# Optimization experiments

Hardware: AMD Instinct MI355X
Metric: run time of the kernel (lower is better)

Reference implementation:

```python
import jax, jax.numpy as jnp
import numpy as np

B, H, W, C = 8, 64, 64, 128
L = H * W
NH = 4
HD = C // NH
SCALE = HD ** -0.5
WIN = 8
SHIFT = 4
DEPTH = 2
K = 3
N = WIN * WIN
NW = (H // WIN) * (W // WIN)


def _rel_pos_index(win):
    coords = np.stack(np.meshgrid(np.arange(win), np.arange(win), indexing='ij'))
    cf = coords.reshape(2, -1)
    rel = (cf[:, :, None] - cf[:, None, :]).transpose(1, 2, 0).copy()
    rel[:, :, 0] += win - 1
    rel[:, :, 1] += win - 1
    rel[:, :, 0] *= 2 * win - 1
    return rel.sum(-1)  # (N, N)

REL_IDX = jnp.asarray(_rel_pos_index(WIN).reshape(-1))


def _attn_mask(Hh, Ww, win, shift):
    img = np.zeros((Hh, Ww))
    cnt = 0
    for hs in (slice(0, -win), slice(-win, -shift), slice(-shift, None)):
        for ws in (slice(0, -win), slice(-win, -shift), slice(-shift, None)):
            img[hs, ws] = cnt
            cnt += 1
    mw = img.reshape(Hh // win, win, Ww // win, win).transpose(0, 2, 1, 3).reshape(-1, win * win)
    m = mw[:, None, :] - mw[:, :, None]
    return jnp.asarray(np.where(m != 0, -100.0, 0.0).astype(np.float32))  # (nW, N, N)

ATTN_MASK = _attn_mask(H, W, WIN, SHIFT)


def layer_norm(x, g, b, eps=1e-5):
    mu = x.mean(-1, keepdims=True)
    var = x.var(-1, keepdims=True)
    return (x - mu) / jnp.sqrt(var + eps) * g + b


def window_partition(x, win):
    Bb, Hh, Ww, Cc = x.shape
    x = x.reshape(Bb, Hh // win, win, Ww // win, win, Cc)
    return x.transpose(0, 1, 3, 2, 4, 5).reshape(-1, win, win, Cc)


def window_reverse(wins, win, Hh, Ww):
    Bb = wins.shape[0] // (Hh * Ww // win // win)
    x = wins.reshape(Bb, Hh // win, Ww // win, win, win, -1)
    return x.transpose(0, 1, 3, 2, 4, 5).reshape(Bb, Hh, Ww, -1)


def swin_block(x, shift, n1g, n1b, qkvw, qkvb, rp, pw, pb, n2g, n2b, f1w, f1b, f2w, f2b):
    shortcut = x
    x = layer_norm(x, n1g, n1b).reshape(B, H, W, C)
    if shift > 0:
        x = jnp.roll(x, (-shift, -shift), axis=(1, 2))
    xw = window_partition(x, WIN).reshape(-1, N, C)  # (B*nW, N, C)
    qkv = (xw @ qkvw + qkvb).reshape(-1, N, 3, NH, HD).transpose(2, 0, 3, 1, 4)
    q, k, v = qkv[0] * SCALE, qkv[1], qkv[2]
    attn = jnp.einsum('whnd,whmd->whnm', q, k)  # (B*nW, NH, N, N)
    bias = rp[REL_IDX].reshape(N, N, NH).transpose(2, 0, 1)
    attn = attn + bias[None]
    if shift > 0:
        attn = (attn.reshape(B, NW, NH, N, N) + ATTN_MASK[None, :, None]).reshape(-1, NH, N, N)
    attn = jax.nn.softmax(attn, axis=-1)
    out = jnp.einsum('whnm,whmd->whnd', attn, v).transpose(0, 2, 1, 3).reshape(-1, N, C)
    out = out @ pw + pb
    x = window_reverse(out.reshape(-1, WIN, WIN, C), WIN, H, W)
    if shift > 0:
        x = jnp.roll(x, (shift, shift), axis=(1, 2))
    x = shortcut + x.reshape(B, L, C)
    h = layer_norm(x, n2g, n2b)
    h = jax.nn.gelu(h @ f1w + f1b, approximate=False) @ f2w + f2b
    return x + h


def conv1d(x, w, b):  # x (B,C,L), w (O,I,K)
    y = jax.lax.conv_general_dilated(x, w, (1,), [(K // 2, K // 2)], dimension_numbers=('NCH', 'OIH', 'NCH'))
    return y + b[None, :, None]


def deform_conv1d(xt, off_w, off_b, msk_w, msk_b):
    x = xt.transpose(0, 2, 1)  # (B, C, L)
    offset = conv1d(x, off_w, off_b)                    # (B, K, L)
    mask = jax.nn.sigmoid(conv1d(x, msk_w, msk_b))      # (B, K, L)
    i = jnp.arange(L, dtype=x.dtype)
    pos = jnp.clip(i[None, None, :] + offset, 0.0, L - 1)  # (B, K, L)
    fp = jnp.floor(pos).astype(jnp.int32)
    cp = jnp.minimum(fp + 1, L - 1)
    alpha = pos - fp.astype(x.dtype)
    idx_f = jnp.broadcast_to(fp[:, None], (B, C, K, L))
    idx_c = jnp.broadcast_to(cp[:, None], (B, C, K, L))
    xe = jnp.broadcast_to(x[:, :, None, :], (B, C, K, L))
    xf = jnp.take_along_axis(xe, idx_f, axis=3)
    xc = jnp.take_along_axis(xe, idx_c, axis=3)
    samp = xf * (1.0 - alpha[:, None]) + xc * alpha[:, None]
    out = (samp * mask[:, None]).sum(2)  # (B, C, L)
    # faithful to torch: output.view(B, L, out_channels) reinterprets memory, no transpose
    return out.reshape(B, L, C)


def _forward(xt, hx, cx, red_w, red_b, n1g, n1b, qkvw, qkvb, rp, pw, pb, n2g, n2b,
             f1w, f1b, f2w, f2b, off_w, off_b, msk_w, msk_b, lf_w, lf_b, gf_w, gf_b, ff_w, ff_b):
    # global branch: inject hidden state then W-MSA / SW-MSA blocks
    g = jnp.concatenate([xt, hx], axis=-1) @ red_w + red_b
    for i, shift in enumerate((0, SHIFT)):
        g = swin_block(g, shift, n1g[i], n1b[i], qkvw[i], qkvb[i], rp[i], pw[i], pb[i],
                       n2g[i], n2b[i], f1w[i], f1b[i], f2w[i], f2b[i])
    # local branch: deformable 1D conv over token axis
    local = deform_conv1d(xt, off_w, off_b, msk_w, msk_b)
    # local-global fusion
    fu = jax.nn.relu((local @ lf_w + lf_b) * (g @ gf_w + gf_b)) @ ff_w + ff_b
    # LSTM-style gating (SwinLSTM cell update)
    gate = jax.nn.sigmoid(fu)
    cell = jnp.tanh(fu)
    cy = gate * (cx + cell)
    hy = gate * jnp.tanh(cy)
    return hy


def setup_inputs():
    key = jax.random.key(0)
    ks = iter(jax.random.split(key, 24))
    def rn(shape, s=0.02):
        return jax.random.normal(next(ks), shape, jnp.float32) * s
    return dict(
        xt=jax.random.normal(next(ks), (B, L, C), jnp.float32),
        hx=jax.random.normal(next(ks), (B, L, C), jnp.float32),
        cx=jax.random.normal(next(ks), (B, L, C), jnp.float32),
        red_w=rn((2 * C, C)), red_b=jnp.zeros((C,), jnp.float32),
        n1g=jnp.ones((DEPTH, C), jnp.float32), n1b=jnp.zeros((DEPTH, C), jnp.float32),
        qkvw=rn((DEPTH, C, 3 * C)), qkvb=jnp.zeros((DEPTH, 3 * C), jnp.float32),
        rp=rn((DEPTH, (2 * WIN - 1) ** 2, NH)),
        pw=rn((DEPTH, C, C)), pb=jnp.zeros((DEPTH, C), jnp.float32),
        n2g=jnp.ones((DEPTH, C), jnp.float32), n2b=jnp.zeros((DEPTH, C), jnp.float32),
        f1w=rn((DEPTH, C, 4 * C)), f1b=jnp.zeros((DEPTH, 4 * C), jnp.float32),
        f2w=rn((DEPTH, 4 * C, C)), f2b=jnp.zeros((DEPTH, C), jnp.float32),
        off_w=rn((K, C, K)), off_b=jnp.zeros((K,), jnp.float32),
        msk_w=rn((K, C, K)), msk_b=jnp.zeros((K,), jnp.float32),
        lf_w=rn((C, C)), lf_b=jnp.zeros((C,), jnp.float32),
        gf_w=rn((C, C)), gf_b=jnp.zeros((C,), jnp.float32),
        ff_w=rn((C, C)), ff_b=jnp.zeros((C,), jnp.float32),
    )


def reference(xt, hx, cx, red_w, red_b, n1g, n1b, qkvw, qkvb, rp, pw, pb, n2g, n2b,
              f1w, f1b, f2w, f2b, off_w, off_b, msk_w, msk_b, lf_w, lf_b, gf_w, gf_b, ff_w, ff_b):
    return _forward(xt, hx, cx, red_w, red_b, n1g, n1b, qkvw, qkvb, rp, pw, pb, n2g, n2b,
                    f1w, f1b, f2w, f2b, off_w, off_b, msk_w, msk_b, lf_w, lf_b, gf_w, gf_b, ff_w, ff_b)
```

## Files before the change

### kernel.cpp

```cpp
#include <hip/hip_runtime.h>
#include <hip/hip_bf16.h>
#include <math.h>

typedef __hip_bfloat16 bf16;
typedef unsigned short u16;
#define BF(x) __bfloat162float(x)
static __device__ __forceinline__ bf16 FB(float x) { return __float2bfloat16(x); }
static __device__ __forceinline__ u16 FBu(float x) {
    bf16 b = __float2bfloat16(x);
    return *(u16*)&b;
}

typedef __attribute__((ext_vector_type(4))) float f32x4;
typedef __attribute__((ext_vector_type(8))) __bf16 bf16x8;


#define O_REDW 0
#define O_QKVW 32768
#define O_PW   131072
#define O_F1W  163840
#define O_F2W  294912
#define O_LFW  425984
#define O_GFW  442368
#define O_FFW  458752
#define O_REDB 475136
#define O_QKVB 475264
#define O_PB   476032
#define O_F1B  476288
#define O_F2B  477312
#define O_LFB  477568
#define O_GFB  477696
#define O_FFB  477824
#define O_RP   477952
#define O_N1G  479752
#define O_N1B  480008
#define O_N2G  480264
#define O_N2B  480520
#define O_OW   480776
#define O_OB   481928
#define O_MW   481931
#define O_MB   483083

#define ROW_S 36
#define CH_S  2320
#define CH32_S 1168

__device__ __forceinline__ int get_mode(const void* xt) {
    const unsigned* w = (const unsigned*)xt;
    int zlo = 0, inband = 0;
    #pragma unroll
    for (int i = 0; i < 32; ++i) {
        unsigned lo = w[i] & 0xFFFFu;
        int e = (int)((lo >> 7) & 0xFF);
        zlo += (lo == 0u || lo == 0x8000u);
        inband += (e >= 100 && e <= 140);
    }
    if (zlo >= 29) return 1;
    return (inband >= 20) ? 0 : 1;
}

__device__ __forceinline__ float LD(const void* p, size_t i, int mode) {
    return mode ? ((const float*)p)[i] : BF(((const bf16*)p)[i]);
}

__device__ __forceinline__ void async16(const u16* g, u16* l) {
    __builtin_amdgcn_global_load_lds(
        (const __attribute__((address_space(1))) unsigned int*)g,
        (__attribute__((address_space(3))) unsigned int*)l, 16, 0, 0);
}

struct PrepT { const void* src; int srcOff, K, N, dstOff; };
struct Prep { PrepT d[29]; int start[30]; };

__global__ void prep_k(Prep p, bf16* __restrict__ dst, const void* __restrict__ dtp) {
    const int mode = get_mode(dtp);
    int i = blockIdx.x * 256 + threadIdx.x;
    if (i >= p.start[29]) return;
    int s = 0;
    while (p.start[s + 1] <= i) ++s;
    int e = i - p.start[s];
    float v;
    if (p.d[s].N > 0) {
        int n = e / p.d[s].K, k = e % p.d[s].K;
        v = LD(p.d[s].src, (size_t)p.d[s].srcOff + (size_t)k * p.d[s].N + n, mode);
    } else {
        v = LD(p.d[s].src, (size_t)p.d[s].srcOff + e, mode);
    }
    dst[p.d[s].dstOff + e] = FB(v);
}

__launch_bounds__(256)
__global__ void redgemm_k(const void* __restrict__ xt, const void* __restrict__ hx,
                          const u16* __restrict__ Bt, const bf16* __restrict__ bias,
                          float* __restrict__ outf) {
    __shared__ __align__(16) u16 Als[2][2048];
    __shared__ __align__(16) u16 Bls[2][4096];
    const int mode = get_mode(xt);
    const int tid = threadIdx.x;
    const int wave = tid >> 6, lane = tid & 63;
    const int q = lane >> 4, lr = lane & 15;
    const int wm = (wave >> 1) << 5, wn = (wave & 1) << 6;
    const int bm = blockIdx.x << 6;
    const int K = 256;
    const f32x4 zero = {0.f, 0.f, 0.f, 0.f};
    f32x4 acc[2][4];
    #pragma unroll
    for (int i = 0; i < 2; ++i)
        #pragma unroll
        for (int j = 0; j < 4; ++j) acc[i][j] = zero;

    const int arow = bm + (tid >> 2);
    const int ksub = (tid & 3) << 3;

    if (mode) {
        float av[8];
        {
            const float* s = (const float*)xt + (size_t)arow * 128 + ksub;
            float4 a = *(const float4*)s; float4 b = *(const float4*)(s + 4);
            av[0]=a.x; av[1]=a.y; av[2]=a.z; av[3]=a.w;
            av[4]=b.x; av[5]=b.y; av[6]=b.z; av[7]=b.w;
            #pragma unroll
            for (int c2 = tid; c2 < 512; c2 += 256)
                async16(Bt + (size_t)(c2 >> 2) * K + ((c2 & 3) << 3), Bls[0] + (c2 << 3));
            u16 o[8];
            #pragma unroll
            for (int e = 0; e < 8; ++e) o[e] = FBu(av[e]);
            *(uint4*)(Als[0] + (tid << 3)) = *(const uint4*)o;
        }
        __syncthreads();
        for (int i = 0; i < 8; ++i) {
            const int cur = i & 1, nxt = cur ^ 1;
            float nv[8];
            if (i < 7) {
                int k1 = (i + 1) << 5;
                const float* s = (const float*)(k1 < 128 ? xt : hx)
                                 + (size_t)arow * 128 + (k1 & 127) + ksub;
                float4 a = *(const float4*)s; float4 b = *(const float4*)(s + 4);
                nv[0]=a.x; nv[1]=a.y; nv[2]=a.z; nv[3]=a.w;
                nv[4]=b.x; nv[5]=b.y; nv[6]=b.z; nv[7]=b.w;
                #pragma unroll
                for (int c2 = tid; c2 < 512; c2 += 256)
                    async16(Bt + (size_t)(c2 >> 2) * K + k1 + ((c2 & 3) << 3),
                            Bls[nxt] + (c2 << 3));
            }
            bf16x8 af[2], bfr[4];
            #pragma unroll
            for (int t = 0; t < 2; ++t)
                af[t] = *(const bf16x8*)(Als[cur] + ((wm + (t << 4) + lr) << 5) + (q << 3));
            #pragma unroll
            for (int t = 0; t < 4; ++t)
                bfr[t] = *(const bf16x8*)(Bls[cur] + ((wn + (t << 4) + lr) << 5) + (q << 3));
            #pragma unroll
            for (int mt = 0; mt < 2; ++mt)
                #pragma unroll
                for (int nt = 0; nt < 4; ++nt)
                    acc[mt][nt] = __builtin_amdgcn_mfma_f32_16x16x32_bf16(
                        af[mt], bfr[nt], acc[mt][nt], 0, 0, 0);
            if (i < 7) {
                u16 o[8];
                #pragma unroll
                for (int e = 0; e < 8; ++e) o[e] = FBu(nv[e]);
                *(uint4*)(Als[nxt] + (tid << 3)) = *(const uint4*)o;
            }
            __syncthreads();
        }
    } else {
        {
            async16((const u16*)xt + (size_t)arow * 128 + ksub, Als[0] + (tid << 3));
            #pragma unroll
            for (int c2 = tid; c2 < 512; c2 += 256)
                async16(Bt + (size_t)(c2 >> 2) * K + ((c2 & 3) << 3), Bls[0] + (c2 << 3));
        }
        __syncthreads();
        for (int i = 0; i < 8; ++i) {
            const int cur = i & 1, nxt = cur ^ 1;
            if (i < 7) {
                int k1 = (i + 1) << 5;
                const u16* s = (const u16*)(k1 < 128 ? xt : hx)
                               + (size_t)arow * 128 + (k1 & 127) + ksub;
                async16(s, Als[nxt] + (tid << 3));
                #pragma unroll
                for (int c2 = tid; c2 < 512; c2 += 256)
                    async16(Bt + (size_t)(c2 >> 2) * K + k1 + ((c2 & 3) << 3),
                            Bls[nxt] + (c2 << 3));
            }
            bf16x8 af[2], bfr[4];
            #pragma unroll
            for (int t = 0; t < 2; ++t)
                af[t] = *(const bf16x8*)(Als[cur] + ((wm + (t << 4) + lr) << 5) + (q << 3));
            #pragma unroll
            for (int t = 0; t < 4; ++t)
                bfr[t] = *(const bf16x8*)(Bls[cur] + ((wn + (t << 4) + lr) << 5) + (q << 3));
            #pragma unroll
            for (int mt = 0; mt < 2; ++mt)
                #pragma unroll
                for (int nt = 0; nt < 4; ++nt)
                    acc[mt][nt] = __builtin_amdgcn_mfma_f32_16x16x32_bf16(
                        af[mt], bfr[nt], acc[mt][nt], 0, 0, 0);
            __syncthreads();
        }
    }

    #pragma unroll
    for (int nt = 0; nt < 4; ++nt) {
        int col = wn + (nt << 4) + lr;
        float bv = BF(bias[col]);
        #pragma unroll
        for (int mt = 0; mt < 2; ++mt) {
            int row0 = bm + wm + (mt << 4) + (q << 2);
            #pragma unroll
            for (int i = 0; i < 4; ++i)
                outf[(size_t)(row0 + i) * 128 + col] = acc[mt][nt][i] + bv;
        }
    }
}

__launch_bounds__(256)
__global__ void qkvln_k(const float* __restrict__ g, const u16* __restrict__ wtu,
                        const bf16* __restrict__ wtb, u16* __restrict__ qkv,
                        int d, int shift) {
    __shared__ __align__(16) u16 Ach[4 * CH_S];
    __shared__ __align__(16) u16 Bb[2][8192];
    const int tid = threadIdx.x;
    const int wave = tid >> 6, lane = tid & 63;
    const int q = lane >> 4, lr = lane & 15;
    const int wm = (wave >> 1) << 5, wn = (wave & 1) << 6;
    const int bm = blockIdx.x << 6;
    const u16* Wq = wtu + O_QKVW + d * 49152;

    #pragma unroll
    for (int i = tid; i < 1024; i += 256) {
        int kc = i >> 9, c = i & 511;
        async16(Wq + (size_t)(c >> 2) * 128 + (kc << 5) + ((c & 3) << 3),
                Bb[0] + (kc << 12) + (c << 3));
    }

    {
        int row = tid >> 2, qtr = tid & 3;
        int r = bm + row;
        int b = r >> 12, rem = r & 4095;
        int wi = rem >> 6, n = rem & 63;
        int hp = ((wi >> 3) << 3) + (n >> 3);
        int wp = ((wi & 7) << 3) + (n & 7);
        int h = (hp + shift) & 63, w = (wp + shift) & 63;
        int src = (b << 12) + (h << 6) + w;
        const float* gr = g + (size_t)src * 128 + qtr * 32;
        float vals[32];
        float s1 = 0.f, s2 = 0.f;
        #pragma unroll
        for (int i = 0; i < 8; ++i) {
            float4 v4 = *(const float4*)(gr + i * 4);
            vals[i * 4] = v4.x; vals[i * 4 + 1] = v4.y;
            vals[i * 4 + 2] = v4.z; vals[i * 4 + 3] = v4.w;
            s1 += v4.x + v4.y + v4.z + v4.w;
            s2 += v4.x * v4.x + v4.y * v4.y + v4.z * v4.z + v4.w * v4.w;
        }
        s1 += __shfl_xor(s1, 1); s1 += __shfl_xor(s1, 2);
        s2 += __shfl_xor(s2, 1); s2 += __shfl_xor(s2, 2);
        float mu = s1 * (1.f / 128.f);
        float var = s2 * (1.f / 128.f) - mu * mu;
        float inv = rsqrtf(var + 1e-5f);
        #pragma unroll
        for (int i = 0; i < 32; ++i) {
            int c = qtr * 32 + i;
            float o = (vals[i] - mu) * inv * BF(wtb[O_N1G + d * 128 + c])
                      + BF(wtb[O_N1B + d * 128 + c]);
            Ach[qtr * CH_S + row * ROW_S + i] = FBu(o);
        }
    }
    __syncthreads();

    const f32x4 zero = {0.f, 0.f, 0.f, 0.f};
    f32x4 acc[2][4];
    for (int s = 0; s < 6; ++s) {
        const int nc = s >> 1, kh = s & 1;
        const int bsel = s & 1;
        if (s < 5) {
            int t = s + 1, nct = t >> 1, kht = t & 1;
            const u16* Bg = Wq + nct * 16384;
            #pragma unroll
            for (int i = tid; i < 1024; i += 256) {
                int kc = i >> 9, c = i & 511;
                async16(Bg + (size_t)(c >> 2) * 128 + (kht << 6) + (kc << 5) + ((c & 3) << 3),
                        Bb[t & 1] + (kc << 12) + (c << 3));
            }
        }
        if (kh == 0) {
            #pragma unroll
            for (int i = 0; i < 2; ++i)
                #pragma unroll
                for (int j = 0; j < 4; ++j) acc[i][j] = zero;
        }
        #pragma unroll
        for (int kc = 0; kc < 2; ++kc) {
            bf16x8 af[2], bfr[4];
            #pragma unroll
            for (int t = 0; t < 2; ++t)
                af[t] = *(const bf16x8*)(Ach + (2 * kh + kc) * CH_S + (wm + (t << 4) + lr) * ROW_S + (q << 3));
            #pragma unroll
            for (int t = 0; t < 4; ++t)
                bfr[t] = *(const bf16x8*)(Bb[bsel] + (kc << 12) + ((wn + (t << 4) + lr) << 5) + (q << 3));
            #pragma unroll
            for (int mt = 0; mt < 2; ++mt)
                #pragma unroll
                for (int nt = 0; nt < 4; ++nt)
                    acc[mt][nt] = __builtin_amdgcn_mfma_f32_16x16x32_bf16(
                        af[mt], bfr[nt], acc[mt][nt], 0, 0, 0);
        }
        if (kh == 1) {
            #pragma unroll
            for (int nt = 0; nt < 4; ++nt) {
                int col = wn + (nt << 4) + lr;
                float bv = BF(wtb[O_QKVB + d * 384 + nc * 128 + col]);
                #pragma unroll
                for (int mt = 0; mt < 2; ++mt) {
                    #pragma unroll
                    for (int i = 0; i < 4; ++i) {
                        int r = bm + wm + (mt << 4) + (q << 2) + i;
                        qkv[(size_t)r * 384 + nc * 128 + col] = FBu(acc[mt][nt][i] + bv);
                    }
                }
            }
        }
        if (s < 5) __syncthreads();
    }
}

__launch_bounds__(256, 2)
__global__ void attn_k(const u16* __restrict__ qkv, const u16* __restrict__ wtu,
                       const bf16* __restrict__ wtb, float* __restrict__ g,
                       int d, int shift) {
    __shared__ __align__(16) u16 vT[4][32][72];
    __shared__ __align__(16) u16 pbuf[4][4608];
    const bf16* rp = wtb + O_RP + d * 900;
    const int wq = blockIdx.x;
    const int head = threadIdx.x >> 6;
    const int lane = threadIdx.x & 63;
    const int q8 = lane >> 4, lr = lane & 15;
    const size_t base = (size_t)wq * 64;
    const f32x4 zero = {0.f, 0.f, 0.f, 0.f};

    #pragma unroll
    for (int j = 0; j < 4; ++j) {
        bf16x8 vv = *(const bf16x8*)(qkv + (base + lane) * 384 + 256 + head * 32 + j * 8);
        #pragma unroll
        for (int e = 0; e < 8; ++e) vT[head][j * 8 + e][lane] = ((const u16*)&vv)[e];
    }

    bf16x8 af[4], bfk[4];
    #pragma unroll
    for (int t = 0; t < 4; ++t) {
        af[t]  = *(const bf16x8*)(qkv + (base + t * 16 + lr) * 384 + head * 32 + q8 * 8);
        bfk[t] = *(const bf16x8*)(qkv + (base + t * 16 + lr) * 384 + 128 + head * 32 + q8 * 8);
    }
    f32x4 accs[4][4];
    #pragma unroll
    for (int rt = 0; rt < 4; ++rt)
        #pragma unroll
        for (int ct = 0; ct < 4; ++ct) accs[rt][ct] = zero;
    #pragma unroll
    for (int rt = 0; rt < 4; ++rt)
        #pragma unroll
        for (int ct = 0; ct < 4; ++ct)
            accs[rt][ct] = __builtin_amdgcn_mfma_f32_16x16x32_bf16(
                af[rt], bfk[ct], accs[rt][ct], 0, 0, 0);

    const int wloc = wq & 63;
    const int wh = (wloc >> 3) << 3, wwb = (wloc & 7) << 3;
    #pragma unroll
    for (int rt = 0; rt < 4; ++rt) {
        #pragma unroll
        for (int i = 0; i < 4; ++i) {
            int r = rt * 16 + q8 * 4 + i;
            int ti = r >> 3, tj = r & 7;
            int regt = 0;
            if (shift) {
                int hp = wh + ti, wp = wwb + tj;
                int rh = hp < 56 ? 0 : (hp < 60 ? 1 : 2);
                int rw = wp < 56 ? 0 : (wp < 60 ? 1 : 2);
                regt = rh * 3 + rw;
            }
            float sv[4];
            float mx = -1e30f;
            #pragma unroll
            for (int ct = 0; ct < 4; ++ct) {
                int m = ct * 16 + lr;
                float a = accs[rt][ct][i] * 0.17677669529663687f;
                int idx = (ti - (m >> 3) + 7) * 15 + (tj - (m & 7) + 7);
                a += BF(rp[idx * 4 + head]);
                if (shift) {
                    int hp = wh + (m >> 3), wp = wwb + (m & 7);
                    int rh = hp < 56 ? 0 : (hp < 60 ? 1 : 2);
                    int rw = wp < 56 ? 0 : (wp < 60 ? 1 : 2);
                    if (regt != rh * 3 + rw) a -= 100.f;
                }
                sv[ct] = a;
                mx = fmaxf(mx, a);
            }
            mx = fmaxf(mx, __shfl_xor(mx, 1));
            mx = fmaxf(mx, __shfl_xor(mx, 2));
            mx = fmaxf(mx, __shfl_xor(mx, 4));
            mx = fmaxf(mx, __shfl_xor(mx, 8));
            float l = 0.f;
            #pragma unroll
            for (int ct = 0; ct < 4; ++ct) { sv[ct] = expf(sv[ct] - mx); l += sv[ct]; }
            l += __shfl_xor(l, 1); l += __shfl_xor(l, 2);
            l += __shfl_xor(l, 4); l += __shfl_xor(l, 8);
            float inv = 1.f / l;
            #pragma unroll
            for (int ct = 0; ct < 4; ++ct)
                pbuf[head][r * 72 + ct * 16 + lr] = FBu(sv[ct] * inv);
        }
    }

    f32x4 acco[4][2];
    #pragma unroll
    for (int rt = 0; rt < 4; ++rt) { acco[rt][0] = zero; acco[rt][1] = zero; }
    #pragma unroll
    for (int mh = 0; mh < 2; ++mh) {
        bf16x8 vb[2];
        #pragma unroll
        for (int dt = 0; dt < 2; ++dt)
            vb[dt] = *(const bf16x8*)(&vT[head][dt * 16 + lr][mh * 32 + q8 * 8]);
        #pragma unroll
        for (int rt = 0; rt < 4; ++rt) {
            bf16x8 pa = *(const bf16x8*)(&pbuf[head][(rt * 16 + lr) * 72 + mh * 32 + q8 * 8]);
            #pragma unroll
            for (int dt = 0; dt < 2; ++dt)
                acco[rt][dt] = __builtin_amdgcn_mfma_f32_16x16x32_bf16(
                    pa, vb[dt], acco[rt][dt], 0, 0, 0);
        }
    }

    #pragma unroll
    for (int rt = 0; rt < 4; ++rt)
        #pragma unroll
        for (int dt = 0; dt < 2; ++dt)
            #pragma unroll
            for (int i = 0; i < 4; ++i) {
                int r = rt * 16 + q8 * 4 + i;
                pbuf[head][r * ROW_S + dt * 16 + lr] = FBu(acco[rt][dt][i]);
            }
    __syncthreads();

    const u16* Wp = wtu + O_PW + d * 16384;
    const int wn = head << 5;
    f32x4 accp[4][2];
    #pragma unroll
    for (int rt = 0; rt < 4; ++rt) { accp[rt][0] = zero; accp[rt][1] = zero; }
    #pragma unroll
    for (int k0 = 0; k0 < 4; ++k0) {
        bf16x8 ap[4], bp[2];
        #pragma unroll
        for (int rt = 0; rt < 4; ++rt)
            ap[rt] = *(const bf16x8*)(&pbuf[k0][(rt * 16 + lr) * ROW_S + q8 * 8]);
        #pragma unroll
        for (int nt = 0; nt < 2; ++nt)
            bp[nt] = *(const bf16x8*)(Wp + (size_t)(wn + (nt << 4) + lr) * 128 + (k0 << 5) + (q8 << 3));
        #pragma unroll
        for (int rt = 0; rt < 4; ++rt)
            #pragma unroll
            for (int nt = 0; nt < 2; ++nt)
                accp[rt][nt] = __builtin_amdgcn_mfma_f32_16x16x32_bf16(
                    ap[rt], bp[nt], accp[rt][nt], 0, 0, 0);
    }
    #pragma unroll
    for (int nt = 0; nt < 2; ++nt) {
        int col = wn + (nt << 4) + lr;
        float bv = BF(wtb[O_PB + d * 128 + col]);
        #pragma unroll
        for (int rt = 0; rt < 4; ++rt) {
            #pragma unroll
            for (int i = 0; i < 4; ++i) {
                int r = (int)base + rt * 16 + q8 * 4 + i;
                float v = accp[rt][nt][i] + bv;
                int b = r >> 12, rem = r & 4095;
                int wi = rem >> 6, n = rem & 63;
                int hp = ((wi >> 3) << 3) + (n >> 3);
                int wp = ((wi & 7) << 3) + (n & 7);
                int h = (hp + shift) & 63, w = (wp + shift) & 63;
                g[((size_t)((b << 12) + (h << 6) + w)) * 128 + col] += v;
            }
        }
    }
}

__launch_bounds__(256)
__global__ void mlp_k(float* __restrict__ g, bf16* __restrict__ gbf,
                      const u16* __restrict__ wtu, const bf16* __restrict__ wtb,
                      int d) {
    __shared__ __align__(16) u16 Ach[4 * CH_S];
    __shared__ __align__(16) u16 bufB1[8192];
    __shared__ __align__(16) u16 bufB2[8192];
    __shared__ __align__(16) u16 buf2[2 * CH_S];
    const int tid = threadIdx.x;
    const int wave = tid >> 6, lane = tid & 63;
    const int q = lane >> 4, lr = lane & 15;
    const int wm = (wave >> 1) << 5;
    const int wn0 = (wave & 1) << 5;
    const int wn = (wave & 1) << 6;
    const int bm = blockIdx.x << 6;

    {
        const u16* B1g = wtu + O_F1W + d * 65536;
        #pragma unroll
        for (int i = tid; i < 1024; i += 256) {
            int kc = i >> 8, c = i & 255;
            async16(B1g + (c >> 2) * 128 + (kc << 5) + ((c & 3) << 3),
                    bufB1 + (kc << 11) + (c << 3));
        }
    }

    {
        int row = tid >> 2, qtr = tid & 3;
        const float* gr = g + (size_t)(bm + row) * 128 + qtr * 32;
        float vals[32];
        float s1 = 0.f, s2 = 0.f;
        #pragma unroll
        for (int i = 0; i < 8; ++i) {
            float4 v4 = *(const float4*)(gr + i * 4);
            vals[i * 4] = v4.x; vals[i * 4 + 1] = v4.y;
            vals[i * 4 + 2] = v4.z; vals[i * 4 + 3] = v4.w;
            s1 += v4.x + v4.y + v4.z + v4.w;
            s2 += v4.x * v4.x + v4.y * v4.y + v4.z * v4.z + v4.w * v4.w;
        }
        s1 += __shfl_xor(s1, 1); s1 += __shfl_xor(s1, 2);
        s2 += __shfl_xor(s2, 1); s2 += __shfl_xor(s2, 2);
        float mu = s1 * (1.f / 128.f);
        float var = s2 * (1.f / 128.f) - mu * mu;
        float inv = rsqrtf(var + 1e-5f);
        #pragma unroll
        for (int i = 0; i < 32; ++i) {
            int c = qtr * 32 + i;
            float o = (vals[i] - mu) * inv * BF(wtb[O_N2G + d * 128 + c])
                      + BF(wtb[O_N2B + d * 128 + c]);
            Ach[qtr * CH_S + row * ROW_S + i] = FBu(o);
        }
    }
    __syncthreads();

    const f32x4 zero = {0.f, 0.f, 0.f, 0.f};
    f32x4 acc2[2][4];
    #pragma unroll
    for (int i = 0; i < 2; ++i)
        #pragma unroll
        for (int j = 0; j < 4; ++j) acc2[i][j] = zero;

    for (int h = 0; h < 8; ++h) {
        {
            const u16* B2g = wtu + O_F2W + d * 65536 + h * 64;
            #pragma unroll
            for (int i = tid; i < 1024; i += 256) {
                int kc = i >> 9, c = i & 511;
                async16(B2g + (size_t)(c >> 2) * 512 + (kc << 5) + ((c & 3) << 3),
                        bufB2 + (kc << 12) + (c << 3));
            }
        }
        f32x4 acc1[2][2];
        #pragma unroll
        for (int i = 0; i < 2; ++i) { acc1[i][0] = zero; acc1[i][1] = zero; }
        #pragma unroll
        for (int k0 = 0; k0 < 4; ++k0) {
            bf16x8 af[2], bfr[2];
            #pragma unroll
            for (int t = 0; t < 2; ++t) {
                af[t]  = *(const bf16x8*)(Ach + k0 * CH_S + (wm + (t << 4) + lr) * ROW_S + (q << 3));
                bfr[t] = *(const bf16x8*)(bufB1 + (k0 << 11) + ((wn0 + (t << 4) + lr) << 5) + (q << 3));
            }
            #pragma unroll
            for (int mt = 0; mt < 2; ++mt)
                #pragma unroll
                for (int nt = 0; nt < 2; ++nt)
                    acc1[mt][nt] = __builtin_amdgcn_mfma_f32_16x16x32_bf16(
                        af[mt], bfr[nt], acc1[mt][nt], 0, 0, 0);
        }
        #pragma unroll
        for (int nt = 0; nt < 2; ++nt) {
            int c = wn0 + (nt << 4) + lr;
            float hb = BF(wtb[O_F1B + d * 512 + h * 64 + c]);
            #pragma unroll
            for (int mt = 0; mt < 2; ++mt) {
                #pragma unroll
                for (int i = 0; i < 4; ++i) {
                    int r = wm + (mt << 4) + (q << 2) + i;
                    float v = acc1[mt][nt][i] + hb;
                    float ge = 0.5f * v * (1.0f + erff(v * 0.70710678118654752f));
                    buf2[(c >> 5) * CH_S + r * ROW_S + (c & 31)] = FBu(ge);
                }
            }
        }
        __syncthreads();
        if (h < 7) {
            const u16* B1g = wtu + O_F1W + d * 65536 + (h + 1) * 8192;
            #pragma unroll
            for (int i = tid; i < 1024; i += 256) {
                int kc = i >> 8, c = i & 255;
                async16(B1g + (c >> 2) * 128 + (kc << 5) + ((c & 3) << 3),
                        bufB1 + (kc << 11) + (c << 3));
            }
        }
        #pragma unroll
        for (int kc = 0; kc < 2; ++kc) {
            bf16x8 ah[2], b2[4];
            #pragma unroll
            for (int t = 0; t < 2; ++t)
                ah[t] = *(const bf16x8*)(buf2 + kc * CH_S + (wm + (t << 4) + lr) * ROW_S + (q << 3));
            #pragma unroll
            for (int t = 0; t < 4; ++t)
                b2[t] = *(const bf16x8*)(bufB2 + (kc << 12) + ((wn + (t << 4) + lr) << 5) + (q << 3));
            #pragma unroll
            for (int mt = 0; mt < 2; ++mt)
                #pragma unroll
                for (int nt = 0; nt < 4; ++nt)
                    acc2[mt][nt] = __builtin_amdgcn_mfma_f32_16x16x32_bf16(
                        ah[mt], b2[nt], acc2[mt][nt], 0, 0, 0);
        }
        __syncthreads();
    }
    #pragma unroll
    for (int nt = 0; nt < 4; ++nt) {
        int col = wn + (nt << 4) + lr;
        float bv = BF(wtb[O_F2B + d * 128 + col]);
        #pragma unroll
        for (int mt = 0; mt < 2; ++mt) {
            #pragma unroll
            for (int i = 0; i < 4; ++i) {
                int r = bm + wm + (mt << 4) + (q << 2) + i;
                size_t idx = (size_t)r * 128 + col;
                float nv = g[idx] + acc2[mt][nt][i] + bv;
                g[idx] = nv;
                if (gbf) gbf[idx] = FB(nv);
            }
        }
    }
}

__launch_bounds__(256, 4)
__global__ void fuse3_k(const u16* __restrict__ Aloc, const u16* __restrict__ Ag,
                        const u16* __restrict__ wtu, const bf16* __restrict__ wtb,
                        const void* __restrict__ cx, void* __restrict__ out,
                        const void* __restrict__ dtp) {
    __shared__ __align__(16) u16 relb[4 * CH32_S];
    const int mode = get_mode(dtp);
    const int tid = threadIdx.x;
    const int wave = tid >> 6, lane = tid & 63;
    const int q = lane >> 4, lr = lane & 15;
    const int wn = wave << 5;
    const int bm = blockIdx.x << 5;
    const f32x4 zero = {0.f, 0.f, 0.f, 0.f};
    f32x4 acc1[2][2], acc2[2][2];
    #pragma unroll
    for (int i = 0; i < 2; ++i)
        #pragma unroll
        for (int j = 0; j < 2; ++j) { acc1[i][j] = zero; acc2[i][j] = zero; }

    #pragma unroll
    for (int k0 = 0; k0 < 4; ++k0) {
        bf16x8 al[2], ag[2], blf[2], bgf[2];
        #pragma unroll
        for (int t = 0; t < 2; ++t) {
            size_t off = (size_t)(bm + (t << 4) + lr) * 128 + (k0 << 5) + (q << 3);
            al[t] = *(const bf16x8*)(Aloc + off);
            ag[t] = *(const bf16x8*)(Ag + off);
        }
        #pragma unroll
        for (int t = 0; t < 2; ++t) {
            int woff = ((wn + (t << 4) + lr) << 7) + (k0 << 5) + (q << 3);
            blf[t] = *(const bf16x8*)(wtu + O_LFW + woff);
            bgf[t] = *(const bf16x8*)(wtu + O_GFW + woff);
        }
        #pragma unroll
        for (int mt = 0; mt < 2; ++mt)
            #pragma unroll
            for (int nt = 0; nt < 2; ++nt) {
                acc1[mt][nt] = __builtin_amdgcn_mfma_f32_16x16x32_bf16(
                    al[mt], blf[nt], acc1[mt][nt], 0, 0, 0);
                acc2[mt][nt] = __builtin_amdgcn_mfma_f32_16x16x32_bf16(
                    ag[mt], bgf[nt], acc2[mt][nt], 0, 0, 0);
            }
    }
    #pragma unroll
    for (int nt = 0; nt < 2; ++nt) {
        int c = wn + (nt << 4) + lr;
        float lfb = BF(wtb[O_LFB + c]);
        float gfb = BF(wtb[O_GFB + c]);
        #pragma unroll
        for (int mt = 0; mt < 2; ++mt) {
            #pragma unroll
            for (int i = 0; i < 4; ++i) {
                int r = (mt << 4) + (q << 2) + i;
                float t1 = acc1[mt][nt][i] + lfb;
                float t2 = acc2[mt][nt][i] + gfb;
                float rel = t1 * t2;
                relb[(c >> 5) * CH32_S + r * ROW_S + (c & 31)] = FBu(rel > 0.f ? rel : 0.f);
            }
        }
    }
    __syncthreads();
    f32x4 acc3[2][2];
    #pragma unroll
    for (int i = 0; i < 2; ++i)
        #pragma unroll
        for (int j = 0; j < 2; ++j) acc3[i][j] = zero;
    #pragma unroll
    for (int k0 = 0; k0 < 4; ++k0) {
        bf16x8 ar[2], bff[2];
        #pragma unroll
        for (int t = 0; t < 2; ++t)
            ar[t] = *(const bf16x8*)(relb + k0 * CH32_S + ((t << 4) + lr) * ROW_S + (q << 3));
        #pragma unroll
        for (int t = 0; t < 2; ++t)
            bff[t] = *(const bf16x8*)(wtu + O_FFW + ((wn + (t << 4) + lr) << 7) + (k0 << 5) + (q << 3));
        #pragma unroll
        for (int mt = 0; mt < 2; ++mt)
            #pragma unroll
            for (int nt = 0; nt < 2; ++nt)
                acc3[mt][nt] = __builtin_amdgcn_mfma_f32_16x16x32_bf16(
                    ar[mt], bff[nt], acc3[mt][nt], 0, 0, 0);
    }
    #pragma unroll
    for (int nt = 0; nt < 2; ++nt) {
        int col = wn + (nt << 4) + lr;
        float ffb = BF(wtb[O_FFB + col]);
        #pragma unroll
        for (int mt = 0; mt < 2; ++mt) {
            #pragma unroll
            for (int i = 0; i < 4; ++i) {
                int r = bm + (mt << 4) + (q << 2) + i;
                size_t idx = (size_t)r * 128 + col;
                float v = acc3[mt][nt][i] + ffb;
                float gate = 1.f / (1.f + expf(-v));
                float cell = tanhf(v);
                float cy = gate * (LD(cx, idx, mode) + cell);
                float hy = gate * tanhf(cy);
                if (mode) ((float*)out)[idx] = hy;
                else      ((bf16*)out)[idx] = FB(hy);
            }
        }
    }
}

__launch_bounds__(256)
__global__ void offmask_k(const void* __restrict__ xt, const bf16* __restrict__ wtb,
                          float4* __restrict__ om) {
    const int mode = get_mode(xt);
    const int wave = threadIdx.x >> 6, lane = threadIdx.x & 63;
    const int gl = blockIdx.x * 4 + wave;
    const int b = gl >> 12, l = gl & 4095;
    float wo[3][3][2], wmk[3][3][2];
    #pragma unroll
    for (int k = 0; k < 3; ++k)
        #pragma unroll
        for (int j = 0; j < 3; ++j) {
            wo[k][j][0]  = BF(wtb[O_OW + (k * 128 + lane) * 3 + j]);
            wo[k][j][1]  = BF(wtb[O_OW + (k * 128 + lane + 64) * 3 + j]);
            wmk[k][j][0] = BF(wtb[O_MW + (k * 128 + lane) * 3 + j]);
            wmk[k][j][1] = BF(wtb[O_MW + (k * 128 + lane + 64) * 3 + j]);
        }
    float a6[6] = {};
    #pragma unroll
    for (int j = 0; j < 3; ++j) {
        int row = l + j - 1;
        if (row >= 0 && row < 4096) {
            size_t base = ((size_t)(b << 12) + row) * 128;
            float x0 = LD(xt, base + lane, mode);
            float x1 = LD(xt, base + lane + 64, mode);
            #pragma unroll
            for (int k = 0; k < 3; ++k) {
                a6[k]     += x0 * wo[k][j][0]  + x1 * wo[k][j][1];
                a6[3 + k] += x0 * wmk[k][j][0] + x1 * wmk[k][j][1];
            }
        }
    }
    #pragma unroll
    for (int off = 32; off > 0; off >>= 1)
        #pragma unroll
        for (int k = 0; k < 6; ++k) a6[k] += __shfl_down(a6[k], off);
    if (lane == 0) {
        #pragma unroll
        for (int k = 0; k < 3; ++k) {
            float off = a6[k] + BF(wtb[O_OB + k]);
            float pos = fminf(fmaxf((float)l + off, 0.f), 4095.f);
            float fpf = floorf(pos);
            float mv = a6[3 + k] + BF(wtb[O_MB + k]);
            float mk = 1.f / (1.f + expf(-mv));
            om[(size_t)gl * 3 + k] = make_float4(fpf, pos - fpf, mk, 0.f);
        }
    }
}

__launch_bounds__(512)
__global__ void sample_k(const void* __restrict__ xt, const float4* __restrict__ om,
                         bf16* __restrict__ outL) {
    __shared__ __align__(16) u16 ot[128 * 72];
    const int mode = get_mode(xt);
    const int tid = threadIdx.x;
    const int b = blockIdx.x >> 6;
    const int l0 = (blockIdx.x & 63) << 6;
    const int c = tid & 127, lh = tid >> 7;
    for (int it = 0; it < 16; ++it) {
        int l_loc = lh * 16 + it;
        size_t gl = (size_t)(b << 12) + l0 + l_loc;
        float o = 0.f;
        #pragma unroll
        for (int k = 0; k < 3; ++k) {
            float4 v = om[gl * 3 + k];
            int fp = (int)v.x;
            int cp = fp + 1 > 4095 ? 4095 : fp + 1;
            float al = v.y, mk = v.z;
            float xf = LD(xt, ((size_t)(b << 12) + fp) * 128 + c, mode);
            float xc = LD(xt, ((size_t)(b << 12) + cp) * 128 + c, mode);
            o += (xf * (1.f - al) + xc * al) * mk;
        }
        ot[c * 72 + l_loc] = FBu(o);
    }
    __syncthreads();
    #pragma unroll
    for (int pass = 0; pass < 2; ++pass) {
        int cc = pass * 64 + (tid >> 3);
        int oo = tid & 7;
        const uint4 v = *(const uint4*)(ot + cc * 72 + oo * 8);
        *(uint4*)(outL + (size_t)b * 524288 + (size_t)cc * 4096 + l0 + oo * 8) = v;
    }
}

extern "C" void kernel_launch(void* const* d_in, const int* in_sizes, int n_in,
                              void* d_out, int out_size, void* d_ws, size_t ws_size,
                              hipStream_t stream) {
    (void)out_size; (void)ws_size;
    int I[28] = {0,1,2,3,4,5,6,7,8,9,10,11,12,13,14,15,16,17,18,19,20,21,22,23,24,25,26,27};
    if (n_in >= 28 && in_sizes[7] != 98304 && in_sizes[23] == 98304 && in_sizes[26] == 1800) {
        int alt[28] = {27, 9, 0, 25, 24, 15, 14, 23, 22, 26, 21, 20, 17, 16,
                       2, 1, 4, 3, 19, 18, 13, 12, 11, 10, 8, 7, 6, 5};
        for (int i = 0; i < 28; ++i) I[i] = alt[i];
    }
    const void* xt = d_in[I[0]];
    const void* hx = d_in[I[1]];
    const void* cx = d_in[I[2]];

    char* wsb = (char*)d_ws;
    float* g    = (float*)wsb;
    u16*   Abf  = (u16*)(wsb + 16777216);
    u16*   Bbf  = (u16*)(wsb + 25165824);
    u16*   Cbf  = (u16*)(wsb + 50331648);
    bf16*  wtb  = (bf16*)(wsb + 58720256);
    u16*   wtu  = (u16*)wtb;
    float4* om  = (float4*)(wsb + 25165824);

    Prep p;
    PrepT descs[29] = {
        {d_in[I[3]],  0,     256, 128, O_REDW},
        {d_in[I[7]],  0,     128, 384, O_QKVW},
        {d_in[I[7]],  49152, 128, 384, O_QKVW + 49152},
        {d_in[I[10]], 0,     128, 128, O_PW},
        {d_in[I[10]], 16384, 128, 128, O_PW + 16384},
        {d_in[I[14]], 0,     128, 512, O_F1W},
        {d_in[I[14]], 65536, 128, 512, O_F1W + 65536},
        {d_in[I[16]], 0,     512, 128, O_F2W},
        {d_in[I[16]], 65536, 512, 128, O_F2W + 65536},
        {d_in[I[22]], 0,     128, 128, O_LFW},
        {d_in[I[24]], 0,     128, 128, O_GFW},
        {d_in[I[26]], 0,     128, 128, O_FFW},
        {d_in[I[4]],  0,  128, 0, O_REDB},
        {d_in[I[8]],  0,  768, 0, O_QKVB},
        {d_in[I[11]], 0,  256, 0, O_PB},
        {d_in[I[15]], 0, 1024, 0, O_F1B},
        {d_in[I[17]], 0,  256, 0, O_F2B},
        {d_in[I[23]], 0,  128, 0, O_LFB},
        {d_in[I[25]], 0,  128, 0, O_GFB},
        {d_in[I[27]], 0,  128, 0, O_FFB},
        {d_in[I[9]],  0, 1800, 0, O_RP},
        {d_in[I[5]],  0,  256, 0, O_N1G},
        {d_in[I[6]],  0,  256, 0, O_N1B},
        {d_in[I[12]], 0,  256, 0, O_N2G},
        {d_in[I[13]], 0,  256, 0, O_N2B},
        {d_in[I[18]], 0, 1152, 0, O_OW},
        {d_in[I[19]], 0,    3, 0, O_OB},
        {d_in[I[20]], 0, 1152, 0, O_MW},
        {d_in[I[21]], 0,    3, 0, O_MB},
    };
    int cum = 0;
    for (int i = 0; i < 29; ++i) {
        p.d[i] = descs[i];
        p.start[i] = cum;
        cum += (descs[i].N > 0) ? descs[i].K * descs[i].N : descs[i].K;
    }
    p.start[29] = cum;

    prep_k<<<(cum + 255) / 256, 256, 0, stream>>>(p, wtb, xt);

    redgemm_k<<<512, 256, 0, stream>>>(xt, hx, wtu + O_REDW, wtb + O_REDB, g);

    for (int d = 0; d < 2; ++d) {
        int shift = d ? 4 : 0;
        qkvln_k<<<512, 256, 0, stream>>>(g, wtu, wtb, Bbf, d, shift);
        attn_k<<<512, 256, 0, stream>>>(Bbf, wtu, wtb, g, d, shift);
        mlp_k<<<512, 256, 0, stream>>>(g, d ? (bf16*)Abf : nullptr, wtu, wtb, d);
    }

    offmask_k<<<8192, 256, 0, stream>>>(xt, wtb, om);
    sample_k<<<512, 512, 0, stream>>>(xt, om, (bf16*)Cbf);
    fuse3_k<<<1024, 256, 0, stream>>>(Cbf, Abf, wtu, wtb, cx, d_out, xt);
}
```

Before: 395.9 us.

## Merge offset/mask and sampling kernels into redgemm and first qkvln launches

The standalone offset/mask kernel now runs as extra blocks of the reduction GEMM launch, and the deformable sampling kernel runs as extra blocks of the first-depth QKV+LayerNorm launch, so independent work shares launches. This removes two kernel launches and lets the small, latency-bound kernels fill otherwise idle CUs alongside the GEMMs. The om buffer moves to a separate workspace offset so it no longer aliases Bbf, which qkvln writes during the same launch. The sampling blocks now run 256 threads with 32 iterations each instead of 512 threads, and the shared memory is unioned, which may change occupancy of the GEMM blocks.

```diff
diff --git a/kernel.cpp b/kernel.cpp
--- a/kernel.cpp
+++ b/kernel.cpp
@@ -90,13 +90,66 @@
 }
 
 __launch_bounds__(256)
-__global__ void redgemm_k(const void* __restrict__ xt, const void* __restrict__ hx,
-                          const u16* __restrict__ Bt, const bf16* __restrict__ bias,
-                          float* __restrict__ outf) {
-    __shared__ __align__(16) u16 Als[2][2048];
-    __shared__ __align__(16) u16 Bls[2][4096];
+__global__ void redoff_k(const void* __restrict__ xt, const void* __restrict__ hx,
+                         const u16* __restrict__ wtu, const bf16* __restrict__ wtb,
+                         float* __restrict__ outf, float4* __restrict__ om) {
+    __shared__ __align__(16) u16 smem[12288];
     const int mode = get_mode(xt);
     const int tid = threadIdx.x;
+
+    if (blockIdx.x >= 512) {
+        const int wave = tid >> 6, lane = tid & 63;
+        const int gl = (blockIdx.x - 512) * 4 + wave;
+        const int b = gl >> 12, l = gl & 4095;
+        float wo[3][3][2], wmk[3][3][2];
+        #pragma unroll
+        for (int k = 0; k < 3; ++k)
+            #pragma unroll
+            for (int j = 0; j < 3; ++j) {
+                wo[k][j][0]  = BF(wtb[O_OW + (k * 128 + lane) * 3 + j]);
+                wo[k][j][1]  = BF(wtb[O_OW + (k * 128 + lane + 64) * 3 + j]);
+                wmk[k][j][0] = BF(wtb[O_MW + (k * 128 + lane) * 3 + j]);
+                wmk[k][j][1] = BF(wtb[O_MW + (k * 128 + lane + 64) * 3 + j]);
+            }
+        float a6[6] = {};
+        #pragma unroll
+        for (int j = 0; j < 3; ++j) {
+            int row = l + j - 1;
+            if (row >= 0 && row < 4096) {
+                size_t base = ((size_t)(b << 12) + row) * 128;
+                float x0 = LD(xt, base + lane, mode);
+                float x1 = LD(xt, base + lane + 64, mode);
+                #pragma unroll
+                for (int k = 0; k < 3; ++k) {
+                    a6[k]     += x0 * wo[k][j][0]  + x1 * wo[k][j][1];
+                    a6[3 + k] += x0 * wmk[k][j][0] + x1 * wmk[k][j][1];
+                }
+            }
+        }
+        #pragma unroll
+        for (int off = 32; off > 0; off >>= 1)
+            #pragma unroll
+            for (int k = 0; k < 6; ++k) a6[k] += __shfl_down(a6[k], off);
+        if (lane == 0) {
+            #pragma unroll
+            for (int k = 0; k < 3; ++k) {
+                float off = a6[k] + BF(wtb[O_OB + k]);
+                float pos = fminf(fmaxf((float)l + off, 0.f), 4095.f);
+                float fpf = floorf(pos);
+                float mv = a6[3 + k] + BF(wtb[O_MB + k]);
+                float mk = 1.f / (1.f + expf(-mv));
+                om[(size_t)gl * 3 + k] = make_float4(fpf, pos - fpf, mk, 0.f);
+            }
+        }
+        return;
+    }
+
+    u16* Als0 = smem;           u16* Als1 = smem + 2048;
+    u16* Bls0 = smem + 4096;    u16* Bls1 = smem + 8192;
+    u16* Als[2] = {Als0, Als1};
+    u16* Bls[2] = {Bls0, Bls1};
+    const u16* Bt = wtu + O_REDW;
+    const bf16* bias = wtb + O_REDB;
     const int wave = tid >> 6, lane = tid & 63;
     const int q = lane >> 4, lr = lane & 15;
     const int wm = (wave >> 1) << 5, wn = (wave & 1) << 6;
@@ -121,11 +174,11 @@
             av[4]=b.x; av[5]=b.y; av[6]=b.z; av[7]=b.w;
             #pragma unroll
             for (int c2 = tid; c2 < 512; c2 += 256)
-                async16(Bt + (size_t)(c2 >> 2) * K + ((c2 & 3) << 3), Bls[0] + (c2 << 3));
+                async16(Bt + (size_t)(c2 >> 2) * K + ((c2 & 3) << 3), Bls0 + (c2 << 3));
             u16 o[8];
             #pragma unroll
             for (int e = 0; e < 8; ++e) o[e] = FBu(av[e]);
-            *(uint4*)(Als[0] + (tid << 3)) = *(const uint4*)o;
+            *(uint4*)(Als0 + (tid << 3)) = *(const uint4*)o;
         }
         __syncthreads();
         for (int i = 0; i < 8; ++i) {
@@ -166,10 +219,10 @@
         }
     } else {
         {
-            async16((const u16*)xt + (size_t)arow * 128 + ksub, Als[0] + (tid << 3));
+            async16((const u16*)xt + (size_t)arow * 128 + ksub, Als0 + (tid << 3));
             #pragma unroll
             for (int c2 = tid; c2 < 512; c2 += 256)
-                async16(Bt + (size_t)(c2 >> 2) * K + ((c2 & 3) << 3), Bls[0] + (c2 << 3));
+                async16(Bt + (size_t)(c2 >> 2) * K + ((c2 & 3) << 3), Bls0 + (c2 << 3));
         }
         __syncthreads();
         for (int i = 0; i < 8; ++i) {
@@ -218,10 +271,47 @@
 __launch_bounds__(256)
 __global__ void qkvln_k(const float* __restrict__ g, const u16* __restrict__ wtu,
                         const bf16* __restrict__ wtb, u16* __restrict__ qkv,
-                        int d, int shift) {
-    __shared__ __align__(16) u16 Ach[4 * CH_S];
-    __shared__ __align__(16) u16 Bb[2][8192];
+                        const void* __restrict__ xt, const float4* __restrict__ om,
+                        bf16* __restrict__ outL, int d, int shift) {
+    __shared__ __align__(16) u16 smem[4 * CH_S + 16384];
     const int tid = threadIdx.x;
+
+    if (blockIdx.x >= 512) {
+        u16* ot = smem;
+        const int mode = get_mode(xt);
+        const int sid = blockIdx.x - 512;
+        const int b = sid >> 6;
+        const int l0 = (sid & 63) << 6;
+        const int c = tid & 127, lh = tid >> 7;
+        for (int it = 0; it < 32; ++it) {
+            int l_loc = lh * 32 + it;
+            size_t gl = (size_t)(b << 12) + l0 + l_loc;
+            float o = 0.f;
+            #pragma unroll
+            for (int k = 0; k < 3; ++k) {
+                float4 v = om[gl * 3 + k];
+                int fp = (int)v.x;
+                int cp = fp + 1 > 4095 ? 4095 : fp + 1;
+                float al = v.y, mk = v.z;
+                float xf = LD(xt, ((size_t)(b << 12) + fp) * 128 + c, mode);
+                float xc = LD(xt, ((size_t)(b << 12) + cp) * 128 + c, mode);
+                o += (xf * (1.f - al) + xc * al) * mk;
+            }
+            ot[c * 72 + l_loc] = FBu(o);
+        }
+        __syncthreads();
+        #pragma unroll
+        for (int pass = 0; pass < 4; ++pass) {
+            int cc = pass * 32 + (tid >> 3);
+            int oo = tid & 7;
+            const uint4 v = *(const uint4*)(ot + cc * 72 + oo * 8);
+            *(uint4*)(outL + (size_t)b * 524288 + (size_t)cc * 4096 + l0 + oo * 8) = v;
+        }
+        return;
+    }
+
+    u16* Ach = smem;
+    u16* Bbp[2] = {smem + 4 * CH_S, smem + 4 * CH_S + 8192};
     const int wave = tid >> 6, lane = tid & 63;
     const int q = lane >> 4, lr = lane & 15;
     const int wm = (wave >> 1) << 5, wn = (wave & 1) << 6;
@@ -232,7 +322,7 @@
     for (int i = tid; i < 1024; i += 256) {
         int kc = i >> 9, c = i & 511;
         async16(Wq + (size_t)(c >> 2) * 128 + (kc << 5) + ((c & 3) << 3),
-                Bb[0] + (kc << 12) + (c << 3));
+                Bbp[0] + (kc << 12) + (c << 3));
     }
 
     {
@@ -282,7 +372,7 @@
             for (int i = tid; i < 1024; i += 256) {
                 int kc = i >> 9, c = i & 511;
                 async16(Bg + (size_t)(c >> 2) * 128 + (kht << 6) + (kc << 5) + ((c & 3) << 3),
-                        Bb[t & 1] + (kc << 12) + (c << 3));
+                        Bbp[t & 1] + (kc << 12) + (c << 3));
             }
         }
         if (kh == 0) {
@@ -299,7 +389,7 @@
                 af[t] = *(const bf16x8*)(Ach + (2 * kh + kc) * CH_S + (wm + (t << 4) + lr) * ROW_S + (q << 3));
             #pragma unroll
             for (int t = 0; t < 4; ++t)
-                bfr[t] = *(const bf16x8*)(Bb[bsel] + (kc << 12) + ((wn + (t << 4) + lr) << 5) + (q << 3));
+                bfr[t] = *(const bf16x8*)(Bbp[bsel] + (kc << 12) + ((wn + (t << 4) + lr) << 5) + (q << 3));
             #pragma unroll
             for (int mt = 0; mt < 2; ++mt)
                 #pragma unroll
@@ -740,90 +830,6 @@
     }
 }
 
-__launch_bounds__(256)
-__global__ void offmask_k(const void* __restrict__ xt, const bf16* __restrict__ wtb,
-                          float4* __restrict__ om) {
-    const int mode = get_mode(xt);
-    const int wave = threadIdx.x >> 6, lane = threadIdx.x & 63;
-    const int gl = blockIdx.x * 4 + wave;
-    const int b = gl >> 12, l = gl & 4095;
-    float wo[3][3][2], wmk[3][3][2];
-    #pragma unroll
-    for (int k = 0; k < 3; ++k)
-        #pragma unroll
-        for (int j = 0; j < 3; ++j) {
-            wo[k][j][0]  = BF(wtb[O_OW + (k * 128 + lane) * 3 + j]);
-            wo[k][j][1]  = BF(wtb[O_OW + (k * 128 + lane + 64) * 3 + j]);
-            wmk[k][j][0] = BF(wtb[O_MW + (k * 128 + lane) * 3 + j]);
-            wmk[k][j][1] = BF(wtb[O_MW + (k * 128 + lane + 64) * 3 + j]);
-        }
-    float a6[6] = {};
-    #pragma unroll
-    for (int j = 0; j < 3; ++j) {
-        int row = l + j - 1;
-        if (row >= 0 && row < 4096) {
-            size_t base = ((size_t)(b << 12) + row) * 128;
-            float x0 = LD(xt, base + lane, mode);
-            float x1 = LD(xt, base + lane + 64, mode);
-            #pragma unroll
-            for (int k = 0; k < 3; ++k) {
-                a6[k]     += x0 * wo[k][j][0]  + x1 * wo[k][j][1];
-                a6[3 + k] += x0 * wmk[k][j][0] + x1 * wmk[k][j][1];
-            }
-        }
-    }
-    #pragma unroll
-    for (int off = 32; off > 0; off >>= 1)
-        #pragma unroll
-        for (int k = 0; k < 6; ++k) a6[k] += __shfl_down(a6[k], off);
-    if (lane == 0) {
-        #pragma unroll
-        for (int k = 0; k < 3; ++k) {
-            float off = a6[k] + BF(wtb[O_OB + k]);
-            float pos = fminf(fmaxf((float)l + off, 0.f), 4095.f);
-            float fpf = floorf(pos);
-            float mv = a6[3 + k] + BF(wtb[O_MB + k]);
-            float mk = 1.f / (1.f + expf(-mv));
-            om[(size_t)gl * 3 + k] = make_float4(fpf, pos - fpf, mk, 0.f);
-        }
-    }
-}
-
-__launch_bounds__(512)
-__global__ void sample_k(const void* __restrict__ xt, const float4* __restrict__ om,
-                         bf16* __restrict__ outL) {
-    __shared__ __align__(16) u16 ot[128 * 72];
-    const int mode = get_mode(xt);
-    const int tid = threadIdx.x;
-    const int b = blockIdx.x >> 6;
-    const int l0 = (blockIdx.x & 63) << 6;
-    const int c = tid & 127, lh = tid >> 7;
-    for (int it = 0; it < 16; ++it) {
-        int l_loc = lh * 16 + it;
-        size_t gl = (size_t)(b << 12) + l0 + l_loc;
-        float o = 0.f;
-        #pragma unroll
-        for (int k = 0; k < 3; ++k) {
-            float4 v = om[gl * 3 + k];
-            int fp = (int)v.x;
-            int cp = fp + 1 > 4095 ? 4095 : fp + 1;
-            float al = v.y, mk = v.z;
-            float xf = LD(xt, ((size_t)(b << 12) + fp) * 128 + c, mode);
-            float xc = LD(xt, ((size_t)(b << 12) + cp) * 128 + c, mode);
-            o += (xf * (1.f - al) + xc * al) * mk;
-        }
-        ot[c * 72 + l_loc] = FBu(o);
-    }
-    __syncthreads();
-    #pragma unroll
-    for (int pass = 0; pass < 2; ++pass) {
-        int cc = pass * 64 + (tid >> 3);
-        int oo = tid & 7;
-        const uint4 v = *(const uint4*)(ot + cc * 72 + oo * 8);
-        *(uint4*)(outL + (size_t)b * 524288 + (size_t)cc * 4096 + l0 + oo * 8) = v;
-    }
-}
-
 extern "C" void kernel_launch(void* const* d_in, const int* in_sizes, int n_in,
                               void* d_out, int out_size, void* d_ws, size_t ws_size,
                               hipStream_t stream) {
@@ -845,7 +851,7 @@
     u16*   Cbf  = (u16*)(wsb + 50331648);
     bf16*  wtb  = (bf16*)(wsb + 58720256);
     u16*   wtu  = (u16*)wtb;
-    float4* om  = (float4*)(wsb + 25165824);
+    float4* om  = (float4*)(wsb + 67108864);
 
     Prep p;
     PrepT descs[29] = {
@@ -889,16 +895,15 @@
 
     prep_k<<<(cum + 255) / 256, 256, 0, stream>>>(p, wtb, xt);
 
-    redgemm_k<<<512, 256, 0, stream>>>(xt, hx, wtu + O_REDW, wtb + O_REDB, g);
+    redoff_k<<<8704, 256, 0, stream>>>(xt, hx, wtu, wtb, g, om);
 
     for (int d = 0; d < 2; ++d) {
         int shift = d ? 4 : 0;
-        qkvln_k<<<512, 256, 0, stream>>>(g, wtu, wtb, Bbf, d, shift);
+        int grid = d ? 512 : 1024;
+        qkvln_k<<<grid, 256, 0, stream>>>(g, wtu, wtb, Bbf, xt, om, (bf16*)Cbf, d, shift);
         attn_k<<<512, 256, 0, stream>>>(Bbf, wtu, wtb, g, d, shift);
         mlp_k<<<512, 256, 0, stream>>>(g, d ? (bf16*)Abf : nullptr, wtu, wtb, d);
     }
 
-    offmask_k<<<8192, 256, 0, stream>>>(xt, wtb, om);
-    sample_k<<<512, 512, 0, stream>>>(xt, om, (bf16*)Cbf);
     fuse3_k<<<1024, 256, 0, stream>>>(Cbf, Abf, wtu, wtb, cx, d_out, xt);
 }
```

After: 423.5 us. 1.07x slower.
